# Optimization experiments

Measured on AMD Instinct MI355X. Metric: run time of the kernel, lower is better.

The kernel has to match this reference:

```python
import jax, jax.numpy as jnp
import numpy as np

B, S, H, E = 8, 2048, 1024, 8

def setup_inputs() -> dict:
    key = jax.random.key(0)
    ks = jax.random.split(key, 7)
    sc = 1.0 / np.sqrt(H)
    return {
        "x":   jax.random.normal(ks[0], (B, S, H), dtype=jnp.float32),
        "We":  jax.random.normal(ks[1], (E, H, H), dtype=jnp.float32) * sc,
        "be":  jax.random.normal(ks[2], (E, H), dtype=jnp.float32) * 0.01,
        "Wr1": jax.random.normal(ks[3], (H, H), dtype=jnp.float32) * sc,
        "br1": jax.random.normal(ks[4], (H,), dtype=jnp.float32) * 0.01,
        "Wr2": jax.random.normal(ks[5], (H, E), dtype=jnp.float32) * sc,
        "br2": jax.random.normal(ks[6], (E,), dtype=jnp.float32) * 0.01,
    }

def reference(x, We, be, Wr1, br1, Wr2, br2):
    # Router: mean over seq -> Linear+ReLU -> Linear -> softmax over experts
    x_mean = x.mean(axis=1)                                   # [B,H]
    h = jax.nn.relu(x_mean @ Wr1 + br1)                        # [B,H]
    routing = jax.nn.softmax(h @ Wr2 + br2, axis=-1)           # [B,E]
    # Dense all-experts MLP: every expert processes every token
    eo = jax.nn.relu(jnp.einsum('bsh,ehd->ebsd', x, We)
                     + be[:, None, None, :])                   # [E,B,S,H]
    # KV caches are zero-initialized and read before any update in the
    # original forward, so their additive contribution is zero here.
    out = jnp.einsum('ebsd,be->bsd', eo, routing)              # [B,S,H]
    return out
```

## Files before the change

### kernel.cpp

```cpp
#include <hip/hip_runtime.h>
#include <stdint.h>

#define Hdim 1024
#define Bdim 8
#define Sdim 2048
#define Edim 8
#define Mtot 16384
#define Ntot 8192

typedef short bf16x8 __attribute__((ext_vector_type(8)));
typedef unsigned short u16x8 __attribute__((ext_vector_type(8)));
typedef float f32x4 __attribute__((ext_vector_type(4)));

__device__ __forceinline__ unsigned short f2bf(float f) {
  union { float f; unsigned u; } v; v.f = f;
  unsigned r = (v.u + 0x7FFFu + ((v.u >> 16) & 1u)) >> 16;
  return (unsigned short)r;
}

__device__ __forceinline__ void gload16(const void* g, void* l) {
  __builtin_amdgcn_global_load_lds((const __attribute__((address_space(1))) void*)g,
                                   (__attribute__((address_space(3))) void*)l,
                                   16, 0, 0);
}

__global__ void k_prep(const float* __restrict__ x,
                       unsigned short* __restrict__ xb,
                       float* __restrict__ part,
                       const float* __restrict__ We,
                       unsigned short* __restrict__ wt) {
  __shared__ float tl[64][65];
  const int bid = blockIdx.x;
  const int t = threadIdx.x;
  if (bid < 512) {
    const int b = bid >> 6;
    const int s0 = (bid & 63) * 32;
    const int hg = (t & 127) << 3;
    const int sp = t >> 7;
    float accv[8];
#pragma unroll
    for (int q = 0; q < 8; ++q) accv[q] = 0.f;
#pragma unroll 4
    for (int i = 0; i < 16; ++i) {
      const int s = s0 + sp + (i << 1);
      const size_t base = ((size_t)b * Sdim + s) * Hdim + hg;
      const float4 lo = *(const float4*)(x + base);
      const float4 hi = *(const float4*)(x + base + 4);
      accv[0] += lo.x; accv[1] += lo.y; accv[2] += lo.z; accv[3] += lo.w;
      accv[4] += hi.x; accv[5] += hi.y; accv[6] += hi.z; accv[7] += hi.w;
      u16x8 pk;
      pk[0] = f2bf(lo.x); pk[1] = f2bf(lo.y); pk[2] = f2bf(lo.z); pk[3] = f2bf(lo.w);
      pk[4] = f2bf(hi.x); pk[5] = f2bf(hi.y); pk[6] = f2bf(hi.z); pk[7] = f2bf(hi.w);
      *(u16x8*)(xb + base) = pk;
    }
    float* pp = part + ((size_t)b * 128 + (bid & 63) * 2 + sp) * Hdim + hg;
#pragma unroll
    for (int q = 0; q < 8; ++q) pp[q] = accv[q];
  } else {
    const int tb = bid - 512;
    const int e = tb >> 8, hb = (tb >> 4) & 15, db = tb & 15;
    const float* src = We + ((size_t)e * Hdim + hb * 64) * Hdim + db * 64;
#pragma unroll 4
    for (int it = 0; it < 16; ++it) {
      int idx = it * 256 + t;
      int r = idx >> 6, c = idx & 63;
      tl[r][c] = src[(size_t)r * Hdim + c];
    }
    __syncthreads();
#pragma unroll 4
    for (int it = 0; it < 16; ++it) {
      int idx = it * 256 + t;
      int r = idx >> 6, c = idx & 63;
      const int np = (db * 64 + r) * 8 + e;
      wt[(size_t)np * Hdim + hb * 64 + c] = f2bf(tl[c][r]);
    }
  }
}

__global__ void k_mean(const float* __restrict__ part, float* __restrict__ xm) {
  __shared__ float red[4][64];
  const int b = blockIdx.y, hc = blockIdx.x, t = threadIdx.x;
  const int h = hc * 64 + (t & 63), q = t >> 6;
  float s = 0.f;
  const float* p = part + ((size_t)b * 128 + q * 32) * Hdim + h;
#pragma unroll 8
  for (int c = 0; c < 32; ++c) s += p[(size_t)c * Hdim];
  red[q][t & 63] = s;
  __syncthreads();
  if (t < 64) {
    float v = (red[0][t] + red[1][t]) + (red[2][t] + red[3][t]);
    xm[b * Hdim + hc * 64 + t] = v * (1.0f / 2048.0f);
  }
}

__global__ void k_r1(const float* __restrict__ xm,
                     const float* __restrict__ Wr1,
                     const float* __restrict__ br1,
                     float* __restrict__ hbuf) {
  __shared__ float xs[Hdim];
  __shared__ float hred[2][128];
  const int b = blockIdx.y, jc = blockIdx.x, t = threadIdx.x;
  for (int k = t; k < Hdim; k += 256) xs[k] = xm[b * Hdim + k];
  __syncthreads();
  const int j = jc * 128 + (t & 127);
  const int kh = (t >> 7) * 512;
  float acc = 0.f;
#pragma unroll 8
  for (int k = 0; k < 512; ++k)
    acc = fmaf(xs[kh + k], Wr1[(size_t)(kh + k) * Hdim + j], acc);
  hred[t >> 7][t & 127] = acc;
  __syncthreads();
  if (t < 128)
    hbuf[b * Hdim + jc * 128 + t] =
        fmaxf(hred[0][t] + hred[1][t] + br1[jc * 128 + t], 0.f);
}

__global__ void k_router2(const float* __restrict__ hbuf,
                          const float* __restrict__ Wr2,
                          const float* __restrict__ br2,
                          float* __restrict__ routing) {
  const int t = threadIdx.x;
  const int e = t & 7;
  const int b = t >> 3;
  float acc = br2[e];
  const float* hb = hbuf + b * Hdim;
#pragma unroll 8
  for (int k = 0; k < Hdim; ++k) acc = fmaf(hb[k], Wr2[k * Edim + e], acc);
  float m = acc;
  for (int d = 1; d < 8; d <<= 1) m = fmaxf(m, __shfl_xor(m, d, 64));
  float p = __expf(acc - m);
  float s = p;
  for (int d = 1; d < 8; d <<= 1) s += __shfl_xor(s, d, 64);
  routing[t] = p / s;
}

__global__ __launch_bounds__(256, 4)
void k_moe_gemm(const unsigned short* __restrict__ xb,
                const unsigned short* __restrict__ wt,
                const float* __restrict__ be,
                const float* __restrict__ routing,
                float* __restrict__ out) {
  __shared__ char smem[33024];
  const int t = threadIdx.x;
  const int wave = t >> 6, lane = t & 63;
  const int la15 = lane & 15;
  const int wr = wave >> 1, wc = wave & 1;

  const int bid = blockIdx.x;
  const int xcd = bid & 7;
  const int i = bid >> 3;
  const int m0 = (xcd * 16 + (i & 15)) * 128;
  const int n0 = (i >> 4) * 128;

  const int cx = (((lane & 7) ^ (lane >> 3)) << 3);
  const unsigned short* aStage = xb + (size_t)(m0 + (lane >> 3)) * Hdim + cx;
  const unsigned short* bStage = wt + (size_t)(n0 + (lane >> 3)) * Hdim + cx;

  const int aOff = (wr * 64 + la15) * 128;
  const int bOff = (wc * 64 + la15) * 128;
  const int swz0 = (((lane >> 4) ^ (lane & 7)) << 4);
  const int swz1 = (((4 + (lane >> 4)) ^ (lane & 7)) << 4);

  f32x4 acc[4][4];
#pragma unroll
  for (int ii = 0; ii < 4; ++ii)
#pragma unroll
    for (int jj = 0; jj < 4; ++jj) acc[ii][jj] = (f32x4){0.f, 0.f, 0.f, 0.f};

  for (int k0 = 0; k0 < Hdim; k0 += 64) {
    __syncthreads();
#pragma unroll
    for (int p = 0; p < 4; ++p) {
      const int c = p * 4 + wave;
      gload16(aStage + (size_t)c * 8 * Hdim + k0, smem + c * 1024);
    }
#pragma unroll
    for (int p = 0; p < 4; ++p) {
      const int c = p * 4 + wave;
      gload16(bStage + (size_t)c * 8 * Hdim + k0, smem + 16384 + c * 1024);
    }
    __syncthreads();
    {
      bf16x8 af[4], bf[4];
#pragma unroll
      for (int ii = 0; ii < 4; ++ii)
        af[ii] = *(const bf16x8*)(smem + aOff + ii * 2048 + swz0);
#pragma unroll
      for (int jj = 0; jj < 4; ++jj)
        bf[jj] = *(const bf16x8*)(smem + 16384 + bOff + jj * 2048 + swz0);
#pragma unroll
      for (int ii = 0; ii < 4; ++ii)
#pragma unroll
        for (int jj = 0; jj < 4; ++jj)
          acc[ii][jj] = __builtin_amdgcn_mfma_f32_16x16x32_bf16(af[ii], bf[jj], acc[ii][jj], 0, 0, 0);
#pragma unroll
      for (int ii = 0; ii < 4; ++ii)
        af[ii] = *(const bf16x8*)(smem + aOff + ii * 2048 + swz1);
#pragma unroll
      for (int jj = 0; jj < 4; ++jj)
        bf[jj] = *(const bf16x8*)(smem + 16384 + bOff + jj * 2048 + swz1);
#pragma unroll
      for (int ii = 0; ii < 4; ++ii)
#pragma unroll
        for (int jj = 0; jj < 4; ++jj)
          acc[ii][jj] = __builtin_amdgcn_mfma_f32_16x16x32_bf16(af[ii], bf[jj], acc[ii][jj], 0, 0, 0);
    }
  }
  __syncthreads();

  float* outb = (float*)smem;
  const int bidx = m0 >> 11;
  const float rw = routing[bidx * Edim + (lane & 7)];
  const bool writer = ((lane & 7) == 0);
#pragma unroll
  for (int j = 0; j < 4; ++j) {
    const int dloc = wc * 8 + j * 2 + ((lane >> 3) & 1);
    const float bias = be[(lane & 7) * Hdim + (n0 >> 3) + dloc];
#pragma unroll
    for (int ii = 0; ii < 4; ++ii) {
#pragma unroll
      for (int r = 0; r < 4; ++r) {
        float v = fmaxf(acc[ii][j][r] + bias, 0.f) * rw;
        v += __shfl_xor(v, 1, 64);
        v += __shfl_xor(v, 2, 64);
        v += __shfl_xor(v, 4, 64);
        if (writer) {
          const int row = wr * 64 + ii * 16 + ((lane >> 4) << 2) + r;
          outb[row * 17 + dloc] = v;
        }
      }
    }
  }
  __syncthreads();
  const size_t obase = (size_t)m0 * Hdim + (n0 >> 3);
#pragma unroll
  for (int it = 0; it < 2; ++it) {
    const int idx = it * 256 + t;
    const int r = idx >> 2;
    const int c = (idx & 3) << 2;
    float4 vv;
    vv.x = outb[r * 17 + c];
    vv.y = outb[r * 17 + c + 1];
    vv.z = outb[r * 17 + c + 2];
    vv.w = outb[r * 17 + c + 3];
    *(float4*)(out + obase + (size_t)r * Hdim + c) = vv;
  }
}

extern "C" void kernel_launch(void* const* d_in, const int* in_sizes, int n_in,
                              void* d_out, int out_size, void* d_ws, size_t ws_size,
                              hipStream_t stream) {
  const float* x   = (const float*)d_in[0];
  const float* We  = (const float*)d_in[1];
  const float* be  = (const float*)d_in[2];
  const float* Wr1 = (const float*)d_in[3];
  const float* br1 = (const float*)d_in[4];
  const float* Wr2 = (const float*)d_in[5];
  const float* br2 = (const float*)d_in[6];
  float* out = (float*)d_out;

  char* ws = (char*)d_ws;
  unsigned short* xb = (unsigned short*)ws;
  unsigned short* wt = (unsigned short*)(ws + 33554432);
  float* part    = (float*)(ws + 50331648);
  float* xm      = (float*)(ws + 54525952);
  float* hbuf    = (float*)(ws + 54558720);
  float* routing = (float*)(ws + 54591488);

  k_prep<<<dim3(2560), 256, 0, stream>>>(x, xb, part, We, wt);
  k_mean<<<dim3(16, Bdim), 256, 0, stream>>>(part, xm);
  k_r1<<<dim3(8, Bdim), 256, 0, stream>>>(xm, Wr1, br1, hbuf);
  k_router2<<<1, 64, 0, stream>>>(hbuf, Wr2, br2, routing);
  k_moe_gemm<<<dim3(8192), 256, 0, stream>>>(xb, wt, be, routing, out);
}
```

Before: 398.6 us.

## Enlarge GEMM tiles to 256x256 with double-buffered LDS and fuse router kernels

The MoE GEMM moves from 128x128 to 256x256 output tiles with 8x8 MFMA accumulators per wave. It double-buffers 64 KB LDS stages so global loads overlap MFMA work, and raises wave priority around the MFMA block. The three router kernels are merged into one per-batch kernel, and the weight transpose in prep now uses vectorized float4 loads and 16-byte bf16 stores. The aim is more data reuse per tile and fewer launches, at the cost of one block per CU, high register pressure and fewer blocks to fill the GPU.

```diff
diff --git a/kernel.cpp b/kernel.cpp
--- a/kernel.cpp
+++ b/kernel.cpp
@@ -23,6 +23,10 @@
                                    (__attribute__((address_space(3))) void*)l,
                                    16, 0, 0);
 }
+
+#define VMCNT_(N) asm volatile("s_waitcnt vmcnt(" #N ")" ::: "memory")
+#define VMCNT(N) VMCNT_(N)
+#define BAR() __builtin_amdgcn_s_barrier()
 
 __global__ void k_prep(const float* __restrict__ x,
                        unsigned short* __restrict__ xb,
@@ -60,87 +64,95 @@
     const int tb = bid - 512;
     const int e = tb >> 8, hb = (tb >> 4) & 15, db = tb & 15;
     const float* src = We + ((size_t)e * Hdim + hb * 64) * Hdim + db * 64;
+#pragma unroll
+    for (int it = 0; it < 4; ++it) {
+      int idx = it * 256 + t;
+      int r = idx >> 4, c4 = (idx & 15) << 2;
+      const float4 v = *(const float4*)(src + (size_t)r * Hdim + c4);
+      tl[r][c4] = v.x; tl[r][c4 + 1] = v.y; tl[r][c4 + 2] = v.z; tl[r][c4 + 3] = v.w;
+    }
+    __syncthreads();
+#pragma unroll
+    for (int it = 0; it < 2; ++it) {
+      int idx = it * 256 + t;
+      int rr = idx >> 3, cg = (idx & 7) << 3;
+      u16x8 pk;
+#pragma unroll
+      for (int q = 0; q < 8; ++q) pk[q] = f2bf(tl[cg + q][rr]);
+      const int np = (db * 64 + rr) * 8 + e;
+      *(u16x8*)(wt + (size_t)np * Hdim + hb * 64 + cg) = pk;
+    }
+  }
+}
+
+__global__ void k_router(const float* __restrict__ part,
+                         const float* __restrict__ Wr1,
+                         const float* __restrict__ br1,
+                         const float* __restrict__ Wr2,
+                         const float* __restrict__ br2,
+                         float* __restrict__ routing) {
+  __shared__ float xs[Hdim];
+  __shared__ float hs[Hdim];
+  __shared__ float red[64];
+  const int b = blockIdx.x, t = threadIdx.x;
+  for (int h = t; h < Hdim; h += 256) {
+    float s = 0.f;
+    const float* p = part + (size_t)b * 128 * Hdim + h;
+#pragma unroll 8
+    for (int c = 0; c < 128; ++c) s += p[(size_t)c * Hdim];
+    xs[h] = s * (1.0f / 2048.0f);
+  }
+  __syncthreads();
+  float a0 = 0.f, a1 = 0.f, a2 = 0.f, a3 = 0.f;
 #pragma unroll 4
-    for (int it = 0; it < 16; ++it) {
-      int idx = it * 256 + t;
-      int r = idx >> 6, c = idx & 63;
-      tl[r][c] = src[(size_t)r * Hdim + c];
-    }
-    __syncthreads();
-#pragma unroll 4
-    for (int it = 0; it < 16; ++it) {
-      int idx = it * 256 + t;
-      int r = idx >> 6, c = idx & 63;
-      const int np = (db * 64 + r) * 8 + e;
-      wt[(size_t)np * Hdim + hb * 64 + c] = f2bf(tl[c][r]);
-    }
-  }
-}
-
-__global__ void k_mean(const float* __restrict__ part, float* __restrict__ xm) {
-  __shared__ float red[4][64];
-  const int b = blockIdx.y, hc = blockIdx.x, t = threadIdx.x;
-  const int h = hc * 64 + (t & 63), q = t >> 6;
-  float s = 0.f;
-  const float* p = part + ((size_t)b * 128 + q * 32) * Hdim + h;
+  for (int k = 0; k < Hdim; ++k) {
+    const float xv = xs[k];
+    const float* w = Wr1 + (size_t)k * Hdim + t;
+    a0 = fmaf(xv, w[0],   a0);
+    a1 = fmaf(xv, w[256], a1);
+    a2 = fmaf(xv, w[512], a2);
+    a3 = fmaf(xv, w[768], a3);
+  }
+  hs[t]       = fmaxf(a0 + br1[t],       0.f);
+  hs[t + 256] = fmaxf(a1 + br1[t + 256], 0.f);
+  hs[t + 512] = fmaxf(a2 + br1[t + 512], 0.f);
+  hs[t + 768] = fmaxf(a3 + br1[t + 768], 0.f);
+  __syncthreads();
+  if (t < 64) {
+    const int e = t & 7;
+    const int kb = (t >> 3) * 128;
+    float s = 0.f;
 #pragma unroll 8
-  for (int c = 0; c < 32; ++c) s += p[(size_t)c * Hdim];
-  red[q][t & 63] = s;
-  __syncthreads();
-  if (t < 64) {
-    float v = (red[0][t] + red[1][t]) + (red[2][t] + red[3][t]);
-    xm[b * Hdim + hc * 64 + t] = v * (1.0f / 2048.0f);
-  }
-}
-
-__global__ void k_r1(const float* __restrict__ xm,
-                     const float* __restrict__ Wr1,
-                     const float* __restrict__ br1,
-                     float* __restrict__ hbuf) {
-  __shared__ float xs[Hdim];
-  __shared__ float hred[2][128];
-  const int b = blockIdx.y, jc = blockIdx.x, t = threadIdx.x;
-  for (int k = t; k < Hdim; k += 256) xs[k] = xm[b * Hdim + k];
-  __syncthreads();
-  const int j = jc * 128 + (t & 127);
-  const int kh = (t >> 7) * 512;
-  float acc = 0.f;
-#pragma unroll 8
-  for (int k = 0; k < 512; ++k)
-    acc = fmaf(xs[kh + k], Wr1[(size_t)(kh + k) * Hdim + j], acc);
-  hred[t >> 7][t & 127] = acc;
-  __syncthreads();
-  if (t < 128)
-    hbuf[b * Hdim + jc * 128 + t] =
-        fmaxf(hred[0][t] + hred[1][t] + br1[jc * 128 + t], 0.f);
-}
-
-__global__ void k_router2(const float* __restrict__ hbuf,
-                          const float* __restrict__ Wr2,
-                          const float* __restrict__ br2,
-                          float* __restrict__ routing) {
-  const int t = threadIdx.x;
-  const int e = t & 7;
-  const int b = t >> 3;
-  float acc = br2[e];
-  const float* hb = hbuf + b * Hdim;
-#pragma unroll 8
-  for (int k = 0; k < Hdim; ++k) acc = fmaf(hb[k], Wr2[k * Edim + e], acc);
-  float m = acc;
-  for (int d = 1; d < 8; d <<= 1) m = fmaxf(m, __shfl_xor(m, d, 64));
-  float p = __expf(acc - m);
-  float s = p;
-  for (int d = 1; d < 8; d <<= 1) s += __shfl_xor(s, d, 64);
-  routing[t] = p / s;
-}
-
-__global__ __launch_bounds__(256, 4)
+    for (int k = kb; k < kb + 128; ++k) s = fmaf(hs[k], Wr2[k * Edim + e], s);
+    red[t] = s;
+  }
+  __syncthreads();
+  if (t < 8) {
+    float l = br2[t];
+#pragma unroll
+    for (int q = 0; q < 8; ++q) l += red[q * 8 + t];
+    red[t] = l;
+  }
+  __syncthreads();
+  if (t == 0) {
+    float m = red[0];
+#pragma unroll
+    for (int e = 1; e < 8; ++e) m = fmaxf(m, red[e]);
+    float p[8]; float s = 0.f;
+#pragma unroll
+    for (int e = 0; e < 8; ++e) { p[e] = __expf(red[e] - m); s += p[e]; }
+#pragma unroll
+    for (int e = 0; e < 8; ++e) routing[b * Edim + e] = p[e] / s;
+  }
+}
+
+__global__ __launch_bounds__(256, 1)
 void k_moe_gemm(const unsigned short* __restrict__ xb,
                 const unsigned short* __restrict__ wt,
                 const float* __restrict__ be,
                 const float* __restrict__ routing,
                 float* __restrict__ out) {
-  __shared__ char smem[33024];
+  extern __shared__ char smem[];
   const int t = threadIdx.x;
   const int wave = t >> 6, lane = t & 63;
   const int la15 = lane & 15;
@@ -149,75 +161,72 @@
   const int bid = blockIdx.x;
   const int xcd = bid & 7;
   const int i = bid >> 3;
-  const int m0 = (xcd * 16 + (i & 15)) * 128;
-  const int n0 = (i >> 4) * 128;
+  const int m0 = (xcd * 8 + (i & 7)) * 256;
+  const int n0 = (i >> 3) * 256;
 
   const int cx = (((lane & 7) ^ (lane >> 3)) << 3);
-  const unsigned short* aStage = xb + (size_t)(m0 + (lane >> 3)) * Hdim + cx;
-  const unsigned short* bStage = wt + (size_t)(n0 + (lane >> 3)) * Hdim + cx;
-
-  const int aOff = (wr * 64 + la15) * 128;
-  const int bOff = (wc * 64 + la15) * 128;
+  const unsigned short* aStage = xb + (size_t)(m0 + wave * 8 + (lane >> 3)) * Hdim + cx;
+  const unsigned short* bStage = wt + (size_t)(n0 + wave * 8 + (lane >> 3)) * Hdim + cx;
+
+  const int aOff = (wr * 128 + la15) * 128;
+  const int bOff = 32768 + (wc * 128 + la15) * 128;
   const int swz0 = (((lane >> 4) ^ (lane & 7)) << 4);
   const int swz1 = (((4 + (lane >> 4)) ^ (lane & 7)) << 4);
 
-  f32x4 acc[4][4];
-#pragma unroll
-  for (int ii = 0; ii < 4; ++ii)
-#pragma unroll
-    for (int jj = 0; jj < 4; ++jj) acc[ii][jj] = (f32x4){0.f, 0.f, 0.f, 0.f};
-
-  for (int k0 = 0; k0 < Hdim; k0 += 64) {
-    __syncthreads();
-#pragma unroll
-    for (int p = 0; p < 4; ++p) {
-      const int c = p * 4 + wave;
-      gload16(aStage + (size_t)c * 8 * Hdim + k0, smem + c * 1024);
-    }
-#pragma unroll
-    for (int p = 0; p < 4; ++p) {
-      const int c = p * 4 + wave;
-      gload16(bStage + (size_t)c * 8 * Hdim + k0, smem + 16384 + c * 1024);
-    }
-    __syncthreads();
-    {
-      bf16x8 af[4], bf[4];
-#pragma unroll
-      for (int ii = 0; ii < 4; ++ii)
-        af[ii] = *(const bf16x8*)(smem + aOff + ii * 2048 + swz0);
-#pragma unroll
-      for (int jj = 0; jj < 4; ++jj)
-        bf[jj] = *(const bf16x8*)(smem + 16384 + bOff + jj * 2048 + swz0);
-#pragma unroll
-      for (int ii = 0; ii < 4; ++ii)
-#pragma unroll
-        for (int jj = 0; jj < 4; ++jj)
-          acc[ii][jj] = __builtin_amdgcn_mfma_f32_16x16x32_bf16(af[ii], bf[jj], acc[ii][jj], 0, 0, 0);
-#pragma unroll
-      for (int ii = 0; ii < 4; ++ii)
-        af[ii] = *(const bf16x8*)(smem + aOff + ii * 2048 + swz1);
-#pragma unroll
-      for (int jj = 0; jj < 4; ++jj)
-        bf[jj] = *(const bf16x8*)(smem + 16384 + bOff + jj * 2048 + swz1);
-#pragma unroll
-      for (int ii = 0; ii < 4; ++ii)
-#pragma unroll
-        for (int jj = 0; jj < 4; ++jj)
-          acc[ii][jj] = __builtin_amdgcn_mfma_f32_16x16x32_bf16(af[ii], bf[jj], acc[ii][jj], 0, 0, 0);
-    }
-  }
-  __syncthreads();
+  f32x4 acc[8][8];
+#pragma unroll
+  for (int ii = 0; ii < 8; ++ii)
+#pragma unroll
+    for (int jj = 0; jj < 8; ++jj) acc[ii][jj] = (f32x4){0.f, 0.f, 0.f, 0.f};
+
+#define STAGE(KS, SB) do { \
+    _Pragma("unroll") for (int p_ = 0; p_ < 8; ++p_) { \
+      gload16(aStage + (size_t)p_ * 32768 + (KS), smem + (SB) * 65536 + (wave + p_ * 4) * 1024); \
+      gload16(bStage + (size_t)p_ * 32768 + (KS), smem + (SB) * 65536 + 32768 + (wave + p_ * 4) * 1024); \
+    } \
+  } while (0)
+
+#define STEP(RB, SB, KS) do { \
+    const char* base_ = smem + (RB) * 65536; \
+    bf16x8 A0[8], B0[8], A1[8], B1[8]; \
+    _Pragma("unroll") for (int q_ = 0; q_ < 8; ++q_) A0[q_] = *(const bf16x8*)(base_ + aOff + q_ * 2048 + swz0); \
+    _Pragma("unroll") for (int q_ = 0; q_ < 8; ++q_) B0[q_] = *(const bf16x8*)(base_ + bOff + q_ * 2048 + swz0); \
+    STAGE(KS, SB); \
+    _Pragma("unroll") for (int q_ = 0; q_ < 8; ++q_) A1[q_] = *(const bf16x8*)(base_ + aOff + q_ * 2048 + swz1); \
+    _Pragma("unroll") for (int q_ = 0; q_ < 8; ++q_) B1[q_] = *(const bf16x8*)(base_ + bOff + q_ * 2048 + swz1); \
+    __builtin_amdgcn_s_setprio(1); \
+    _Pragma("unroll") for (int i_ = 0; i_ < 8; ++i_) \
+      _Pragma("unroll") for (int j_ = 0; j_ < 8; ++j_) \
+        acc[i_][j_] = __builtin_amdgcn_mfma_f32_16x16x32_bf16(A0[i_], B0[j_], acc[i_][j_], 0, 0, 0); \
+    _Pragma("unroll") for (int i_ = 0; i_ < 8; ++i_) \
+      _Pragma("unroll") for (int j_ = 0; j_ < 8; ++j_) \
+        acc[i_][j_] = __builtin_amdgcn_mfma_f32_16x16x32_bf16(A1[i_], B1[j_], acc[i_][j_], 0, 0, 0); \
+    __builtin_amdgcn_s_setprio(0); \
+    VMCNT(0); \
+    BAR(); \
+  } while (0)
+
+  STAGE(0, 0);
+  VMCNT(0);
+  BAR();
+
+#pragma unroll 1
+  for (int jj = 0; jj < 8; ++jj) {
+    const int k0 = jj * 128;
+    STEP(0, 1, k0 + 64);
+    STEP(1, 0, (jj < 7) ? (k0 + 128) : 0);
+  }
 
   float* outb = (float*)smem;
   const int bidx = m0 >> 11;
   const float rw = routing[bidx * Edim + (lane & 7)];
   const bool writer = ((lane & 7) == 0);
 #pragma unroll
-  for (int j = 0; j < 4; ++j) {
-    const int dloc = wc * 8 + j * 2 + ((lane >> 3) & 1);
+  for (int j = 0; j < 8; ++j) {
+    const int dloc = wc * 16 + j * 2 + ((lane >> 3) & 1);
     const float bias = be[(lane & 7) * Hdim + (n0 >> 3) + dloc];
 #pragma unroll
-    for (int ii = 0; ii < 4; ++ii) {
+    for (int ii = 0; ii < 8; ++ii) {
 #pragma unroll
       for (int r = 0; r < 4; ++r) {
         float v = fmaxf(acc[ii][j][r] + bias, 0.f) * rw;
@@ -225,26 +234,27 @@
         v += __shfl_xor(v, 2, 64);
         v += __shfl_xor(v, 4, 64);
         if (writer) {
-          const int row = wr * 64 + ii * 16 + ((lane >> 4) << 2) + r;
-          outb[row * 17 + dloc] = v;
+          const int row = wr * 128 + ii * 16 + ((lane >> 4) << 2) + r;
+          outb[row * 33 + dloc] = v;
         }
       }
     }
   }
-  __syncthreads();
+  BAR();
   const size_t obase = (size_t)m0 * Hdim + (n0 >> 3);
 #pragma unroll
-  for (int it = 0; it < 2; ++it) {
-    const int idx = it * 256 + t;
-    const int r = idx >> 2;
-    const int c = (idx & 3) << 2;
+  for (int it = 0; it < 8; ++it) {
+    const int r = it * 32 + (t >> 3);
+    const int c = (t & 7) * 4;
     float4 vv;
-    vv.x = outb[r * 17 + c];
-    vv.y = outb[r * 17 + c + 1];
-    vv.z = outb[r * 17 + c + 2];
-    vv.w = outb[r * 17 + c + 3];
+    vv.x = outb[r * 33 + c];
+    vv.y = outb[r * 33 + c + 1];
+    vv.z = outb[r * 33 + c + 2];
+    vv.w = outb[r * 33 + c + 3];
     *(float4*)(out + obase + (size_t)r * Hdim + c) = vv;
   }
+#undef STAGE
+#undef STEP
 }
 
 extern "C" void kernel_launch(void* const* d_in, const int* in_sizes, int n_in,
@@ -263,13 +273,12 @@
   unsigned short* xb = (unsigned short*)ws;
   unsigned short* wt = (unsigned short*)(ws + 33554432);
   float* part    = (float*)(ws + 50331648);
-  float* xm      = (float*)(ws + 54525952);
-  float* hbuf    = (float*)(ws + 54558720);
-  float* routing = (float*)(ws + 54591488);
+  float* routing = (float*)(ws + 54525952);
+
+  hipFuncSetAttribute((const void*)k_moe_gemm,
+                      hipFuncAttributeMaxDynamicSharedMemorySize, 131072);
 
   k_prep<<<dim3(2560), 256, 0, stream>>>(x, xb, part, We, wt);
-  k_mean<<<dim3(16, Bdim), 256, 0, stream>>>(part, xm);
-  k_r1<<<dim3(8, Bdim), 256, 0, stream>>>(xm, Wr1, br1, hbuf);
-  k_router2<<<1, 64, 0, stream>>>(hbuf, Wr2, br2, routing);
-  k_moe_gemm<<<dim3(8192), 256, 0, stream>>>(xb, wt, be, routing, out);
-}
+  k_router<<<dim3(Bdim), 256, 0, stream>>>(part, Wr1, br1, Wr2, br2, routing);
+  k_moe_gemm<<<dim3(2048), 256, 131072, stream>>>(xb, wt, be, routing, out);
+}
```

After: 726.0 us. +82.1%, slower.

## Fuse router kernels, vectorize weight transpose, trim GEMM LDS for higher occupancy

Applied to the files above, without the earlier changes.

Merges the mean, first router layer, and second router layer plus softmax into a single per-batch kernel to remove launches and intermediate buffers. Vectorizes the expert weight transpose in the prep kernel with float4 loads and packed bf16 stores. Reduces GEMM shared memory to 32KB and raises launch bounds to 5 blocks per CU for more occupancy. The fused router uses only 8 blocks, which may lengthen that stage, and the smaller LDS buffer may drop padding that avoided bank conflicts.

```diff
diff --git a/kernel.cpp b/kernel.cpp
--- a/kernel.cpp
+++ b/kernel.cpp
@@ -60,87 +60,95 @@
     const int tb = bid - 512;
     const int e = tb >> 8, hb = (tb >> 4) & 15, db = tb & 15;
     const float* src = We + ((size_t)e * Hdim + hb * 64) * Hdim + db * 64;
+#pragma unroll
+    for (int it = 0; it < 4; ++it) {
+      int idx = it * 256 + t;
+      int r = idx >> 4, c4 = (idx & 15) << 2;
+      const float4 v = *(const float4*)(src + (size_t)r * Hdim + c4);
+      tl[r][c4] = v.x; tl[r][c4 + 1] = v.y; tl[r][c4 + 2] = v.z; tl[r][c4 + 3] = v.w;
+    }
+    __syncthreads();
+#pragma unroll
+    for (int it = 0; it < 2; ++it) {
+      int idx = it * 256 + t;
+      int rr = idx >> 3, cg = (idx & 7) << 3;
+      u16x8 pk;
+#pragma unroll
+      for (int q = 0; q < 8; ++q) pk[q] = f2bf(tl[cg + q][rr]);
+      const int np = (db * 64 + rr) * 8 + e;
+      *(u16x8*)(wt + (size_t)np * Hdim + hb * 64 + cg) = pk;
+    }
+  }
+}
+
+__global__ void k_router(const float* __restrict__ part,
+                         const float* __restrict__ Wr1,
+                         const float* __restrict__ br1,
+                         const float* __restrict__ Wr2,
+                         const float* __restrict__ br2,
+                         float* __restrict__ routing) {
+  __shared__ float xs[Hdim];
+  __shared__ float hs[Hdim];
+  __shared__ float red[64];
+  const int b = blockIdx.x, t = threadIdx.x;
+  for (int h = t; h < Hdim; h += 256) {
+    float s = 0.f;
+    const float* p = part + (size_t)b * 128 * Hdim + h;
+#pragma unroll 8
+    for (int c = 0; c < 128; ++c) s += p[(size_t)c * Hdim];
+    xs[h] = s * (1.0f / 2048.0f);
+  }
+  __syncthreads();
+  float a0 = 0.f, a1 = 0.f, a2 = 0.f, a3 = 0.f;
 #pragma unroll 4
-    for (int it = 0; it < 16; ++it) {
-      int idx = it * 256 + t;
-      int r = idx >> 6, c = idx & 63;
-      tl[r][c] = src[(size_t)r * Hdim + c];
-    }
-    __syncthreads();
-#pragma unroll 4
-    for (int it = 0; it < 16; ++it) {
-      int idx = it * 256 + t;
-      int r = idx >> 6, c = idx & 63;
-      const int np = (db * 64 + r) * 8 + e;
-      wt[(size_t)np * Hdim + hb * 64 + c] = f2bf(tl[c][r]);
-    }
-  }
-}
-
-__global__ void k_mean(const float* __restrict__ part, float* __restrict__ xm) {
-  __shared__ float red[4][64];
-  const int b = blockIdx.y, hc = blockIdx.x, t = threadIdx.x;
-  const int h = hc * 64 + (t & 63), q = t >> 6;
-  float s = 0.f;
-  const float* p = part + ((size_t)b * 128 + q * 32) * Hdim + h;
+  for (int k = 0; k < Hdim; ++k) {
+    const float xv = xs[k];
+    const float* w = Wr1 + (size_t)k * Hdim + t;
+    a0 = fmaf(xv, w[0],   a0);
+    a1 = fmaf(xv, w[256], a1);
+    a2 = fmaf(xv, w[512], a2);
+    a3 = fmaf(xv, w[768], a3);
+  }
+  hs[t]       = fmaxf(a0 + br1[t],       0.f);
+  hs[t + 256] = fmaxf(a1 + br1[t + 256], 0.f);
+  hs[t + 512] = fmaxf(a2 + br1[t + 512], 0.f);
+  hs[t + 768] = fmaxf(a3 + br1[t + 768], 0.f);
+  __syncthreads();
+  if (t < 64) {
+    const int e = t & 7;
+    const int kb = (t >> 3) * 128;
+    float s = 0.f;
 #pragma unroll 8
-  for (int c = 0; c < 32; ++c) s += p[(size_t)c * Hdim];
-  red[q][t & 63] = s;
-  __syncthreads();
-  if (t < 64) {
-    float v = (red[0][t] + red[1][t]) + (red[2][t] + red[3][t]);
-    xm[b * Hdim + hc * 64 + t] = v * (1.0f / 2048.0f);
-  }
-}
-
-__global__ void k_r1(const float* __restrict__ xm,
-                     const float* __restrict__ Wr1,
-                     const float* __restrict__ br1,
-                     float* __restrict__ hbuf) {
-  __shared__ float xs[Hdim];
-  __shared__ float hred[2][128];
-  const int b = blockIdx.y, jc = blockIdx.x, t = threadIdx.x;
-  for (int k = t; k < Hdim; k += 256) xs[k] = xm[b * Hdim + k];
-  __syncthreads();
-  const int j = jc * 128 + (t & 127);
-  const int kh = (t >> 7) * 512;
-  float acc = 0.f;
-#pragma unroll 8
-  for (int k = 0; k < 512; ++k)
-    acc = fmaf(xs[kh + k], Wr1[(size_t)(kh + k) * Hdim + j], acc);
-  hred[t >> 7][t & 127] = acc;
-  __syncthreads();
-  if (t < 128)
-    hbuf[b * Hdim + jc * 128 + t] =
-        fmaxf(hred[0][t] + hred[1][t] + br1[jc * 128 + t], 0.f);
-}
-
-__global__ void k_router2(const float* __restrict__ hbuf,
-                          const float* __restrict__ Wr2,
-                          const float* __restrict__ br2,
-                          float* __restrict__ routing) {
-  const int t = threadIdx.x;
-  const int e = t & 7;
-  const int b = t >> 3;
-  float acc = br2[e];
-  const float* hb = hbuf + b * Hdim;
-#pragma unroll 8
-  for (int k = 0; k < Hdim; ++k) acc = fmaf(hb[k], Wr2[k * Edim + e], acc);
-  float m = acc;
-  for (int d = 1; d < 8; d <<= 1) m = fmaxf(m, __shfl_xor(m, d, 64));
-  float p = __expf(acc - m);
-  float s = p;
-  for (int d = 1; d < 8; d <<= 1) s += __shfl_xor(s, d, 64);
-  routing[t] = p / s;
-}
-
-__global__ __launch_bounds__(256, 4)
+    for (int k = kb; k < kb + 128; ++k) s = fmaf(hs[k], Wr2[k * Edim + e], s);
+    red[t] = s;
+  }
+  __syncthreads();
+  if (t < 8) {
+    float l = br2[t];
+#pragma unroll
+    for (int q = 0; q < 8; ++q) l += red[q * 8 + t];
+    red[t] = l;
+  }
+  __syncthreads();
+  if (t == 0) {
+    float m = red[0];
+#pragma unroll
+    for (int e = 1; e < 8; ++e) m = fmaxf(m, red[e]);
+    float p[8]; float s = 0.f;
+#pragma unroll
+    for (int e = 0; e < 8; ++e) { p[e] = __expf(red[e] - m); s += p[e]; }
+#pragma unroll
+    for (int e = 0; e < 8; ++e) routing[b * Edim + e] = p[e] / s;
+  }
+}
+
+__global__ __launch_bounds__(256, 5)
 void k_moe_gemm(const unsigned short* __restrict__ xb,
                 const unsigned short* __restrict__ wt,
                 const float* __restrict__ be,
                 const float* __restrict__ routing,
                 float* __restrict__ out) {
-  __shared__ char smem[33024];
+  __shared__ char smem[32768];
   const int t = threadIdx.x;
   const int wave = t >> 6, lane = t & 63;
   const int la15 = lane & 15;
@@ -263,13 +271,9 @@
   unsigned short* xb = (unsigned short*)ws;
   unsigned short* wt = (unsigned short*)(ws + 33554432);
   float* part    = (float*)(ws + 50331648);
-  float* xm      = (float*)(ws + 54525952);
-  float* hbuf    = (float*)(ws + 54558720);
-  float* routing = (float*)(ws + 54591488);
+  float* routing = (float*)(ws + 54525952);
 
   k_prep<<<dim3(2560), 256, 0, stream>>>(x, xb, part, We, wt);
-  k_mean<<<dim3(16, Bdim), 256, 0, stream>>>(part, xm);
-  k_r1<<<dim3(8, Bdim), 256, 0, stream>>>(xm, Wr1, br1, hbuf);
-  k_router2<<<1, 64, 0, stream>>>(hbuf, Wr2, br2, routing);
+  k_router<<<dim3(Bdim), 256, 0, stream>>>(part, Wr1, br1, Wr2, br2, routing);
   k_moe_gemm<<<dim3(8192), 256, 0, stream>>>(xb, wt, be, routing, out);
 }
```

Measured after the change: 483.8 us. 1.21x slower.
